# Performance work log

Hardware: AMD Instinct MI355X
Metric: run time of the kernel (lower is better)

## Reference

```python
import jax, jax.numpy as jnp
import numpy as np

N_NODES = 100000
N_EDGES = 3200000
IN_DIM = 128
OUT_DIM = 128


def setup_inputs() -> dict:
    key = jax.random.key(0)
    k1, k2, k3, k4, k5 = jax.random.split(key, 5)
    features = jax.random.normal(k1, (N_NODES, IN_DIM), dtype=jnp.float32)
    edge_src = jax.random.randint(k2, (N_EDGES,), 0, N_NODES, dtype=jnp.int32)
    edge_dst = jax.random.randint(k3, (N_EDGES,), 0, N_NODES, dtype=jnp.int32)
    edge_vals = jax.random.uniform(k4, (N_EDGES,), dtype=jnp.float32)
    # kaiming_normal_ on [in, out] with fan_in = in
    weight = jax.random.normal(k5, (IN_DIM, OUT_DIM), dtype=jnp.float32) * np.sqrt(2.0 / IN_DIM)
    bias = jnp.zeros((OUT_DIM,), dtype=jnp.float32)
    return {
        "features": features,
        "edge_src": edge_src,
        "edge_dst": edge_dst,
        "edge_vals": edge_vals,
        "weight": weight,
        "bias": bias,
    }


def reference(features, edge_src, edge_dst, edge_vals, weight, bias):
    # h = X @ W  : [N, out]
    h = features @ weight
    # SpMM: out[dst] += A[dst, src] * h[src]   (COO edge-list aggregation)
    msgs = h[edge_src] * edge_vals[:, None]          # [E, out]
    agg = jax.ops.segment_sum(msgs, edge_dst, num_segments=N_NODES)
    return agg + bias
```

## Files before the change

kernel.cpp:

```cpp
#include <hip/hip_runtime.h>

#define IN_DIM 128
#define OUT_DIM 128
#define BIN_SHIFT 9
#define BIN_NODES 512
#define CAP1 18432
#define TILE_A 6144

typedef __attribute__((ext_vector_type(8))) short bf16x8;
typedef __attribute__((ext_vector_type(4))) float f32x4;

__device__ inline unsigned short f2bf(float f) {
    unsigned u = __float_as_uint(f);
    unsigned r = (u + 0x7fff + ((u >> 16) & 1)) >> 16;
    return (unsigned short)r;
}
__device__ inline float bflo(unsigned h) { return __uint_as_float(h << 16); }
__device__ inline float bfhi(unsigned h) { return __uint_as_float(h & 0xffff0000u); }

__global__ __launch_bounds__(256) void zero_ints(int* __restrict__ p, int n) {
    int i = blockIdx.x * 256 + threadIdx.x;
    if (i < n) p[i] = 0;
}

__global__ __launch_bounds__(256) void pack_w(const float* __restrict__ W,
                                              unsigned short* __restrict__ Wpack) {
    int idx = blockIdx.x * 256 + threadIdx.x;
    if (idx >= 16384) return;
    int j = idx & 7;
    int lane = (idx >> 3) & 63;
    int kc = (idx >> 9) & 3;
    int tn = idx >> 11;
    int k = kc * 32 + (lane >> 4) * 8 + j;
    int n = tn * 16 + (lane & 15);
    Wpack[idx] = f2bf(W[k * OUT_DIM + n]);
}

__global__ __launch_bounds__(256) void gemm_mfma(const float* __restrict__ X,
                                                 const unsigned short* __restrict__ Wpack,
                                                 unsigned short* __restrict__ Hb,
                                                 int n_rows) {
    int strip = blockIdx.x * 4 + (threadIdx.x >> 6);
    long long m0 = (long long)strip * 32;
    if (m0 >= n_rows) return;
    int lane = threadIdx.x & 63;
    int quad = lane >> 4;
    int low = lane & 15;

    const bf16x8* B = (const bf16x8*)Wpack;

    long long r0 = m0 + low;
    long long r1 = m0 + 16 + low;
    if (r1 >= n_rows) r1 = n_rows - 1;
    if (r0 >= n_rows) r0 = n_rows - 1;

    f32x4 acc[2][8] = {};

#pragma unroll
    for (int kc = 0; kc < 4; ++kc) {
        const float4* p0 = (const float4*)(X + r0 * IN_DIM + kc * 32 + quad * 8);
        const float4* p1 = (const float4*)(X + r1 * IN_DIM + kc * 32 + quad * 8);
        float4 x0a = p0[0], x0b = p0[1];
        float4 x1a = p1[0], x1b = p1[1];
        bf16x8 afr0, afr1;
        afr0[0] = f2bf(x0a.x); afr0[1] = f2bf(x0a.y); afr0[2] = f2bf(x0a.z); afr0[3] = f2bf(x0a.w);
        afr0[4] = f2bf(x0b.x); afr0[5] = f2bf(x0b.y); afr0[6] = f2bf(x0b.z); afr0[7] = f2bf(x0b.w);
        afr1[0] = f2bf(x1a.x); afr1[1] = f2bf(x1a.y); afr1[2] = f2bf(x1a.z); afr1[3] = f2bf(x1a.w);
        afr1[4] = f2bf(x1b.x); afr1[5] = f2bf(x1b.y); afr1[6] = f2bf(x1b.z); afr1[7] = f2bf(x1b.w);
#pragma unroll
        for (int tn = 0; tn < 8; ++tn) {
            bf16x8 bfr = B[(tn * 4 + kc) * 64 + lane];
            acc[0][tn] = __builtin_amdgcn_mfma_f32_16x16x32_bf16(afr0, bfr, acc[0][tn], 0, 0, 0);
            acc[1][tn] = __builtin_amdgcn_mfma_f32_16x16x32_bf16(afr1, bfr, acc[1][tn], 0, 0, 0);
        }
    }

#pragma unroll
    for (int t = 0; t < 2; ++t) {
#pragma unroll
        for (int tn = 0; tn < 8; ++tn) {
#pragma unroll
            for (int r = 0; r < 4; ++r) {
                long long row = m0 + t * 16 + quad * 4 + r;
                if (row < n_rows) {
                    int col = tn * 16 + low;
                    Hb[row * OUT_DIM + col] = f2bf(acc[t][tn][r]);
                }
            }
        }
    }
}

__global__ __launch_bounds__(1024) void binA(const int* __restrict__ src,
                                             const int* __restrict__ dst,
                                             const float* __restrict__ vals,
                                             int* __restrict__ gcur,
                                             int2* __restrict__ entries,
                                             int n_edges, int nbin) {
    __shared__ int2 eL[TILE_A];
    __shared__ unsigned char bL[TILE_A];
    __shared__ int hist[256];
    __shared__ int dbase[256];

    const int tid = threadIdx.x;
    const int base = blockIdx.x * TILE_A;
    const int n = min(TILE_A, n_edges - base);

    for (int i = tid; i < nbin; i += 1024) hist[i] = 0;
    __syncthreads();

    for (int i = tid; i < n; i += 1024) {
        int d = dst[base + i];
        int s = src[base + i];
        float v = vals[base + i];
        int b = d >> BIN_SHIFT;
        eL[i] = make_int2(s | ((d & (BIN_NODES - 1)) << 17), __float_as_int(v));
        bL[i] = (unsigned char)b;
        atomicAdd(&hist[b], 1);
    }
    __syncthreads();

    for (int l = tid; l < nbin; l += 1024) {
        int c = hist[l];
        dbase[l] = (c > 0) ? atomicAdd(&gcur[l], c) : 0;
        hist[l] = 0;
    }
    __syncthreads();

    for (int i = tid; i < n; i += 1024) {
        int b = bL[i];
        int pos = dbase[b] + atomicAdd(&hist[b], 1);
        if (pos < CAP1) entries[(long long)b * CAP1 + pos] = eL[i];
    }
}

__global__ __launch_bounds__(1024) void binB(const int2* __restrict__ entries,
                                             const int* __restrict__ gcur,
                                             int2* __restrict__ csr,
                                             int2* __restrict__ node_meta,
                                             int n_nodes) {
    __shared__ int hist[BIN_NODES];
    __shared__ int off[BIN_NODES];

    const int bin = blockIdx.x;
    const int tid = threadIdx.x;
    const int cnt = min(gcur[bin], CAP1);
    const long long base = (long long)bin * CAP1;

    for (int i = tid; i < BIN_NODES; i += 1024) hist[i] = 0;
    __syncthreads();

    for (int i = tid; i < cnt; i += 1024) {
        int l = (entries[base + i].x >> 17) & (BIN_NODES - 1);
        atomicAdd(&hist[l], 1);
    }
    __syncthreads();

    if (tid < BIN_NODES) off[tid] = hist[tid];
    __syncthreads();
    for (int d = 1; d < BIN_NODES; d <<= 1) {
        int v = 0;
        if (tid < BIN_NODES && tid >= d) v = off[tid - d];
        __syncthreads();
        if (tid < BIN_NODES) off[tid] += v;
        __syncthreads();
    }
    if (tid < BIN_NODES) {
        int ex = off[tid] - hist[tid];
        int node = bin * BIN_NODES + tid;
        if (node < n_nodes) node_meta[node] = make_int2((int)(base + ex), hist[tid]);
        off[tid] = ex;
    }
    __syncthreads();

    for (int i = tid; i < cnt; i += 1024) {
        int2 e = entries[base + i];
        int l = (e.x >> 17) & (BIN_NODES - 1);
        int pos = atomicAdd(&off[l], 1);
        csr[base + pos] = e;
    }
}

__global__ __launch_bounds__(256) void gather_nodes(
    const int2* __restrict__ node_meta, const int2* __restrict__ csr,
    const unsigned short* __restrict__ Hb, const float* __restrict__ bias,
    float* __restrict__ out, int n_nodes) {
    int node = blockIdx.x * 4 + (threadIdx.x >> 6);
    if (node >= n_nodes) return;
    int lane = threadIdx.x & 63;

    int2 meta = node_meta[node];
    int beg = meta.x;
    int end = meta.x + meta.y;

    float2 acc = ((const float2*)bias)[lane];

    int e = beg;
    for (; e + 4 <= end; e += 4) {
        int2 c0 = csr[e + 0];
        int2 c1 = csr[e + 1];
        int2 c2 = csr[e + 2];
        int2 c3 = csr[e + 3];
        unsigned h0 = *(const unsigned*)(Hb + (long long)(c0.x & 0x1ffff) * OUT_DIM + lane * 2);
        unsigned h1 = *(const unsigned*)(Hb + (long long)(c1.x & 0x1ffff) * OUT_DIM + lane * 2);
        unsigned h2 = *(const unsigned*)(Hb + (long long)(c2.x & 0x1ffff) * OUT_DIM + lane * 2);
        unsigned h3 = *(const unsigned*)(Hb + (long long)(c3.x & 0x1ffff) * OUT_DIM + lane * 2);
        float v0 = __int_as_float(c0.y);
        float v1 = __int_as_float(c1.y);
        float v2 = __int_as_float(c2.y);
        float v3 = __int_as_float(c3.y);
        acc.x += v0 * bflo(h0) + v1 * bflo(h1) + v2 * bflo(h2) + v3 * bflo(h3);
        acc.y += v0 * bfhi(h0) + v1 * bfhi(h1) + v2 * bfhi(h2) + v3 * bfhi(h3);
    }
    for (; e < end; ++e) {
        int2 c0 = csr[e];
        unsigned h0 = *(const unsigned*)(Hb + (long long)(c0.x & 0x1ffff) * OUT_DIM + lane * 2);
        float v0 = __int_as_float(c0.y);
        acc.x += v0 * bflo(h0);
        acc.y += v0 * bfhi(h0);
    }

    ((float2*)(out + (long long)node * OUT_DIM))[lane] = acc;
}

extern "C" void kernel_launch(void* const* d_in, const int* in_sizes, int n_in,
                              void* d_out, int out_size, void* d_ws, size_t ws_size,
                              hipStream_t stream) {
    const float* features  = (const float*)d_in[0];
    const int* edge_src    = (const int*)d_in[1];
    const int* edge_dst    = (const int*)d_in[2];
    const float* edge_vals = (const float*)d_in[3];
    const float* weight    = (const float*)d_in[4];
    const float* bias      = (const float*)d_in[5];

    const int n_nodes = in_sizes[0] / IN_DIM;
    const int n_edges = in_sizes[1];
    const int nbin = (n_nodes + BIN_NODES - 1) / BIN_NODES;

    int2* entries       = (int2*)d_ws;
    int2* csr           = entries + (long long)nbin * CAP1;
    int2* node_meta     = csr + (long long)nbin * CAP1;
    unsigned short* Hb  = (unsigned short*)(node_meta + n_nodes);
    unsigned short* Wp  = Hb + (long long)n_nodes * OUT_DIM;
    int* gcur           = (int*)(Wp + 16384);

    float* out = (float*)d_out;

    zero_ints<<<(nbin + 255) / 256, 256, 0, stream>>>(gcur, nbin);
    pack_w<<<64, 256, 0, stream>>>(weight, Wp);

    binA<<<(n_edges + TILE_A - 1) / TILE_A, 1024, 0, stream>>>(
        edge_src, edge_dst, edge_vals, gcur, entries, n_edges, nbin);

    int n_strips = (n_nodes + 31) / 32;
    gemm_mfma<<<(n_strips + 3) / 4, 256, 0, stream>>>(features, Wp, Hb, n_nodes);

    binB<<<nbin, 1024, 0, stream>>>(entries, gcur, csr, node_meta, n_nodes);

    gather_nodes<<<(n_nodes + 3) / 4, 256, 0, stream>>>(
        node_meta, csr, Hb, bias, out, n_nodes);
}
```

Baseline: 334.2 us.

## Co-schedule edge binning and MFMA GEMM in one interleaved kernel launch

Merges the edge-binning pass and the bf16 MFMA GEMM into a single `phase1` launch. The first blocks alternate between GEMM and binning work, and the remaining blocks do only binning, so the memory-bound scatter and the compute-bound GEMM can occupy the GPU at the same time. The gcur zeroing is folded into the weight-packing kernel to save a launch. Binning tiles drop to 3072 edges with 256-thread blocks to match the GEMM block shape, and the gather loop is unrolled to 8 edges with packed float2 FMAs for more loads in flight. Risks are higher global-atomic traffic on gcur from the larger number of binning blocks, and occupancy limited by the shared-memory struct that GEMM blocks also reserve.

```diff
diff --git a/kernel.cpp b/kernel.cpp
--- a/kernel.cpp
+++ b/kernel.cpp
@@ -5,10 +5,11 @@
 #define BIN_SHIFT 9
 #define BIN_NODES 512
 #define CAP1 18432
-#define TILE_A 6144
+#define TILE_A 3072
 
 typedef __attribute__((ext_vector_type(8))) short bf16x8;
 typedef __attribute__((ext_vector_type(4))) float f32x4;
+typedef __attribute__((ext_vector_type(2))) float f32x2;
 
 __device__ inline unsigned short f2bf(float f) {
     unsigned u = __float_as_uint(f);
@@ -18,14 +19,11 @@
 __device__ inline float bflo(unsigned h) { return __uint_as_float(h << 16); }
 __device__ inline float bfhi(unsigned h) { return __uint_as_float(h & 0xffff0000u); }
 
-__global__ __launch_bounds__(256) void zero_ints(int* __restrict__ p, int n) {
-    int i = blockIdx.x * 256 + threadIdx.x;
-    if (i < n) p[i] = 0;
-}
-
-__global__ __launch_bounds__(256) void pack_w(const float* __restrict__ W,
-                                              unsigned short* __restrict__ Wpack) {
+__global__ __launch_bounds__(256) void pack_w_zero(const float* __restrict__ W,
+                                                   unsigned short* __restrict__ Wpack,
+                                                   int* __restrict__ gcur, int nbin) {
     int idx = blockIdx.x * 256 + threadIdx.x;
+    if (blockIdx.x == 0 && threadIdx.x < nbin) gcur[threadIdx.x] = 0;
     if (idx >= 16384) return;
     int j = idx & 7;
     int lane = (idx >> 3) & 63;
@@ -36,14 +34,70 @@
     Wpack[idx] = f2bf(W[k * OUT_DIM + n]);
 }
 
-__global__ __launch_bounds__(256) void gemm_mfma(const float* __restrict__ X,
-                                                 const unsigned short* __restrict__ Wpack,
-                                                 unsigned short* __restrict__ Hb,
-                                                 int n_rows) {
-    int strip = blockIdx.x * 4 + (threadIdx.x >> 6);
+struct BinSmem {
+    int2 eL[TILE_A];
+    int hist[256];
+    int dbase[256];
+    unsigned char bL[TILE_A];
+};
+
+__global__ __launch_bounds__(256) void phase1(
+    const int* __restrict__ src, const int* __restrict__ dst,
+    const float* __restrict__ vals, int* __restrict__ gcur,
+    int2* __restrict__ entries, int n_edges, int nbin, int nA,
+    const float* __restrict__ X, const unsigned short* __restrict__ Wpack,
+    unsigned short* __restrict__ Hb, int n_rows, int nG) {
+    __shared__ BinSmem sm;
+
+    int b = blockIdx.x;
+    int isGemm, widx;
+    if (b < 2 * nG) {
+        isGemm = (b & 1) == 0;
+        widx = b >> 1;
+    } else {
+        isGemm = 0;
+        widx = nG + (b - 2 * nG);
+    }
+
+    const int tid = threadIdx.x;
+
+    if (!isGemm) {
+        const int base = widx * TILE_A;
+        const int n = min(TILE_A, n_edges - base);
+
+        for (int i = tid; i < nbin; i += 256) sm.hist[i] = 0;
+        __syncthreads();
+
+        for (int i = tid; i < n; i += 256) {
+            int d = dst[base + i];
+            int s = src[base + i];
+            float v = vals[base + i];
+            int bin = d >> BIN_SHIFT;
+            sm.eL[i] = make_int2(s | ((d & (BIN_NODES - 1)) << 17), __float_as_int(v));
+            sm.bL[i] = (unsigned char)bin;
+            atomicAdd(&sm.hist[bin], 1);
+        }
+        __syncthreads();
+
+        for (int l = tid; l < nbin; l += 256) {
+            int c = sm.hist[l];
+            sm.dbase[l] = (c > 0) ? atomicAdd(&gcur[l], c) : 0;
+            sm.hist[l] = 0;
+        }
+        __syncthreads();
+
+        for (int i = tid; i < n; i += 256) {
+            int bin = sm.bL[i];
+            int pos = sm.dbase[bin] + atomicAdd(&sm.hist[bin], 1);
+            if (pos < CAP1) entries[(long long)bin * CAP1 + pos] = sm.eL[i];
+        }
+        return;
+    }
+
+    int strip = widx * 4 + (tid >> 6);
     long long m0 = (long long)strip * 32;
     if (m0 >= n_rows) return;
-    int lane = threadIdx.x & 63;
+    int lane = tid & 63;
     int quad = lane >> 4;
     int low = lane & 15;
 
@@ -91,49 +145,6 @@
     }
 }
 
-__global__ __launch_bounds__(1024) void binA(const int* __restrict__ src,
-                                             const int* __restrict__ dst,
-                                             const float* __restrict__ vals,
-                                             int* __restrict__ gcur,
-                                             int2* __restrict__ entries,
-                                             int n_edges, int nbin) {
-    __shared__ int2 eL[TILE_A];
-    __shared__ unsigned char bL[TILE_A];
-    __shared__ int hist[256];
-    __shared__ int dbase[256];
-
-    const int tid = threadIdx.x;
-    const int base = blockIdx.x * TILE_A;
-    const int n = min(TILE_A, n_edges - base);
-
-    for (int i = tid; i < nbin; i += 1024) hist[i] = 0;
-    __syncthreads();
-
-    for (int i = tid; i < n; i += 1024) {
-        int d = dst[base + i];
-        int s = src[base + i];
-        float v = vals[base + i];
-        int b = d >> BIN_SHIFT;
-        eL[i] = make_int2(s | ((d & (BIN_NODES - 1)) << 17), __float_as_int(v));
-        bL[i] = (unsigned char)b;
-        atomicAdd(&hist[b], 1);
-    }
-    __syncthreads();
-
-    for (int l = tid; l < nbin; l += 1024) {
-        int c = hist[l];
-        dbase[l] = (c > 0) ? atomicAdd(&gcur[l], c) : 0;
-        hist[l] = 0;
-    }
-    __syncthreads();
-
-    for (int i = tid; i < n; i += 1024) {
-        int b = bL[i];
-        int pos = dbase[b] + atomicAdd(&hist[b], 1);
-        if (pos < CAP1) entries[(long long)b * CAP1 + pos] = eL[i];
-    }
-}
-
 __global__ __launch_bounds__(1024) void binB(const int2* __restrict__ entries,
                                              const int* __restrict__ gcur,
                                              int2* __restrict__ csr,
@@ -193,34 +204,40 @@
     int beg = meta.x;
     int end = meta.x + meta.y;
 
-    float2 acc = ((const float2*)bias)[lane];
+    f32x2 acc;
+    {
+        float2 bb = ((const float2*)bias)[lane];
+        acc[0] = bb.x; acc[1] = bb.y;
+    }
 
     int e = beg;
-    for (; e + 4 <= end; e += 4) {
-        int2 c0 = csr[e + 0];
-        int2 c1 = csr[e + 1];
-        int2 c2 = csr[e + 2];
-        int2 c3 = csr[e + 3];
-        unsigned h0 = *(const unsigned*)(Hb + (long long)(c0.x & 0x1ffff) * OUT_DIM + lane * 2);
-        unsigned h1 = *(const unsigned*)(Hb + (long long)(c1.x & 0x1ffff) * OUT_DIM + lane * 2);
-        unsigned h2 = *(const unsigned*)(Hb + (long long)(c2.x & 0x1ffff) * OUT_DIM + lane * 2);
-        unsigned h3 = *(const unsigned*)(Hb + (long long)(c3.x & 0x1ffff) * OUT_DIM + lane * 2);
-        float v0 = __int_as_float(c0.y);
-        float v1 = __int_as_float(c1.y);
-        float v2 = __int_as_float(c2.y);
-        float v3 = __int_as_float(c3.y);
-        acc.x += v0 * bflo(h0) + v1 * bflo(h1) + v2 * bflo(h2) + v3 * bflo(h3);
-        acc.y += v0 * bfhi(h0) + v1 * bfhi(h1) + v2 * bfhi(h2) + v3 * bfhi(h3);
+    for (; e + 8 <= end; e += 8) {
+        int2 c[8];
+#pragma unroll
+        for (int j = 0; j < 8; ++j) c[j] = csr[e + j];
+        unsigned h[8];
+#pragma unroll
+        for (int j = 0; j < 8; ++j)
+            h[j] = *(const unsigned*)(Hb + (long long)(c[j].x & 0x1ffff) * OUT_DIM + lane * 2);
+#pragma unroll
+        for (int j = 0; j < 8; ++j) {
+            float v = __int_as_float(c[j].y);
+            f32x2 hv; hv[0] = bflo(h[j]); hv[1] = bfhi(h[j]);
+            f32x2 vv; vv[0] = v; vv[1] = v;
+            acc += vv * hv;
+        }
     }
     for (; e < end; ++e) {
         int2 c0 = csr[e];
         unsigned h0 = *(const unsigned*)(Hb + (long long)(c0.x & 0x1ffff) * OUT_DIM + lane * 2);
-        float v0 = __int_as_float(c0.y);
-        acc.x += v0 * bflo(h0);
-        acc.y += v0 * bfhi(h0);
-    }
-
-    ((float2*)(out + (long long)node * OUT_DIM))[lane] = acc;
+        float v = __int_as_float(c0.y);
+        f32x2 hv; hv[0] = bflo(h0); hv[1] = bfhi(h0);
+        f32x2 vv; vv[0] = v; vv[1] = v;
+        acc += vv * hv;
+    }
+
+    float2 res; res.x = acc[0]; res.y = acc[1];
+    ((float2*)(out + (long long)node * OUT_DIM))[lane] = res;
 }
 
 extern "C" void kernel_launch(void* const* d_in, const int* in_sizes, int n_in,
@@ -246,14 +263,14 @@
 
     float* out = (float*)d_out;
 
-    zero_ints<<<(nbin + 255) / 256, 256, 0, stream>>>(gcur, nbin);
-    pack_w<<<64, 256, 0, stream>>>(weight, Wp);
-
-    binA<<<(n_edges + TILE_A - 1) / TILE_A, 1024, 0, stream>>>(
-        edge_src, edge_dst, edge_vals, gcur, entries, n_edges, nbin);
-
-    int n_strips = (n_nodes + 31) / 32;
-    gemm_mfma<<<(n_strips + 3) / 4, 256, 0, stream>>>(features, Wp, Hb, n_nodes);
+    pack_w_zero<<<64, 256, 0, stream>>>(weight, Wp, gcur, nbin);
+
+    const int nA = (n_edges + TILE_A - 1) / TILE_A;
+    const int n_strips = (n_nodes + 31) / 32;
+    const int nG = (n_strips + 3) / 4;
+    phase1<<<nA + nG, 256, 0, stream>>>(edge_src, edge_dst, edge_vals, gcur,
+                                        entries, n_edges, nbin, nA,
+                                        features, Wp, Hb, n_nodes, nG);
 
     binB<<<nbin, 1024, 0, stream>>>(entries, gcur, csr, node_meta, n_nodes);
 
```

Measured after the change: 320.7 us. -4.0%, faster.
